# Kernel tuning notes

Hardware: AMD Instinct MI355X
Metric: run time of the kernel (lower is better)

Reference implementation:

```python
import jax, jax.numpy as jnp
import numpy as np

B, D, N_NEG, MAX_N = 4096, 256, 32768, 16
NEG_INF = float(jnp.finfo(jnp.float32).min)

def _l2norm(x):
    return x / jnp.linalg.norm(x, axis=-1, keepdims=True)

def setup_inputs() -> dict:
    key = jax.random.key(0)
    kq, kp, kn = jax.random.split(key, 3)
    q_emb = _l2norm(jax.random.normal(kq, (B, D), dtype=jnp.float32))
    p_emb = _l2norm(jax.random.normal(kp, (B, D), dtype=jnp.float32))
    n_emb = _l2norm(jax.random.normal(kn, (N_NEG, D), dtype=jnp.float32))
    # ragged counts in [0,16], mean 8, summing exactly to N_NEG
    rng = np.random.default_rng(0)
    d = rng.integers(0, 9, size=B // 2)
    counts = np.concatenate([8 + d, 8 - d])
    rng.shuffle(counts)
    n_counts = jnp.asarray(counts, dtype=jnp.int32)
    log_tau = jnp.log(jnp.asarray(0.07, dtype=jnp.float32))
    return {"q_emb": q_emb, "p_emb": p_emb, "n_emb": n_emb,
            "n_counts": n_counts, "log_tau": log_tau}

def reference(q_emb, p_emb, n_emb, n_counts, log_tau):
    Bq = q_emb.shape[0]
    tau = jnp.clip(jnp.exp(log_tau), 1e-4, 1.0)
    sim = (q_emb @ p_emb.T) / tau                      # [B, B]
    n_sim = (q_emb @ n_emb.T) / tau                    # [B, N]
    # vectorized ragged packing: query i's negatives live at
    # n_sim[i, offset[i] : offset[i]+cnt[i]]
    offsets = jnp.cumsum(n_counts) - n_counts          # [B]
    col = offsets[:, None] + jnp.arange(MAX_N)[None, :]
    valid = jnp.arange(MAX_N)[None, :] < n_counts[:, None]
    gathered = jnp.take_along_axis(n_sim, jnp.clip(col, 0, n_sim.shape[1] - 1), axis=1)
    neg_cols = jnp.where(valid, gathered, NEG_INF)     # [B, MAX_N]
    full = jnp.concatenate([sim, neg_cols], axis=1)    # [B, B+MAX_N]
    labels = jnp.arange(Bq)
    logp_q = jax.nn.log_softmax(full, axis=-1)
    loss_q = -jnp.mean(jnp.take_along_axis(logp_q, labels[:, None], axis=1))
    logp_p = jax.nn.log_softmax(sim.T, axis=-1)
    loss_p = -jnp.mean(jnp.take_along_axis(logp_p, labels[:, None], axis=1))
    return (loss_q + loss_p) / 2.0
```

## Files before the change

### kernel.cpp

```cpp
#include <hip/hip_runtime.h>
#include <math.h>

#define BQ 4096
#define DD 256
#define NNEG 32768

typedef __bf16 bf16x8 __attribute__((ext_vector_type(8)));
typedef float f32x4 __attribute__((ext_vector_type(4)));

typedef const __attribute__((address_space(1))) void GvPtr;
typedef __attribute__((address_space(3))) void LdsPtr;


__device__ __forceinline__ float get_inv_tau(const float* __restrict__ lt) {
  float tau = __expf(lt[0]);
  tau = fminf(fmaxf(tau, 1e-4f), 1.0f);
  return 1.0f / tau;
}

__device__ __forceinline__ unsigned int f2bf(float f) {
  unsigned int u = __float_as_uint(f);
  u += 0x7FFFu + ((u >> 16) & 1u);
  return u >> 16;
}

__global__ __launch_bounds__(256) void cvtscan_kernel(
    const float* __restrict__ q, const float* __restrict__ p,
    const int* __restrict__ counts,
    ushort* __restrict__ qb, ushort* __restrict__ pb,
    int* __restrict__ owner, float* __restrict__ rowcol ) {
  __shared__ int wtot[4];
  const int t = threadIdx.x;
  if (blockIdx.x < 1024) {
    const int i = blockIdx.x * 256 + t;
    const int half = (BQ * DD) / 8;
    const float* src = (i < half) ? q : p;
    ushort* dst = (i < half) ? qb : pb;
    const int idx = (i < half) ? i : (i - half);
    const float4 a = *reinterpret_cast<const float4*>(&src[idx * 8]);
    const float4 b = *reinterpret_cast<const float4*>(&src[idx * 8 + 4]);
    uint4 o;
    o.x = f2bf(a.x) | (f2bf(a.y) << 16);
    o.y = f2bf(a.z) | (f2bf(a.w) << 16);
    o.z = f2bf(b.x) | (f2bf(b.y) << 16);
    o.w = f2bf(b.z) | (f2bf(b.w) << 16);
    *reinterpret_cast<uint4*>(&dst[idx * 8]) = o;
    return;
  }
  const int wid = t >> 6, lane = t & 63;
  const float4 z = {0.f, 0.f, 0.f, 0.f};
#pragma unroll
  for (int i = 0; i < 8; ++i) reinterpret_cast<float4*>(rowcol)[t * 8 + i] = z;

  int cl[16];
  int s = 0;
#pragma unroll
  for (int i = 0; i < 4; ++i) {
    const int4 c = reinterpret_cast<const int4*>(counts)[t * 4 + i];
    cl[4 * i + 0] = c.x; cl[4 * i + 1] = c.y; cl[4 * i + 2] = c.z; cl[4 * i + 3] = c.w;
    s += c.x + c.y + c.z + c.w;
  }
  int x = s;
#pragma unroll
  for (int off = 1; off < 64; off <<= 1) {
    const int v = __shfl_up(x, off);
    if (lane >= off) x += v;
  }
  if (lane == 63) wtot[wid] = x;
  __syncthreads();
  int base = 0;
  for (int w = 0; w < wid; ++w) base += wtot[w];
  int running = base + x - s;
#pragma unroll
  for (int k = 0; k < 16; ++k) {
    const int qi = 16 * t + k;
    for (int e = 0; e < cl[k]; ++e) owner[running + e] = qi;
    running += cl[k];
  }
}

__global__ __launch_bounds__(256) void simneg_kernel(
    const ushort* __restrict__ qb, const ushort* __restrict__ pb,
    const float* __restrict__ q, const float* __restrict__ n_emb,
    const int* __restrict__ owner, const float* __restrict__ logtau,
    float* __restrict__ row_sum, float* __restrict__ col_sum,
    float* __restrict__ diag) {
  __shared__ ushort As[2][128 * 32];
  __shared__ ushort Bs[2][128 * 32];

  const int tid = threadIdx.x;
  const float inv_tau = get_inv_tau(logtau);
  const int bid = (int)blockIdx.x;

  if (bid >= 1024) {
    const int j = (bid - 1024) * 32 + (tid >> 3);
    const int sl = tid & 7;
    const int ow = owner[j];
    const float4* nrow = reinterpret_cast<const float4*>(n_emb + (size_t)j * DD);
    const float4* qrow = reinterpret_cast<const float4*>(q + (size_t)ow * DD);
    float d0 = 0.f, d1 = 0.f;
#pragma unroll
    for (int t = 0; t < 8; t += 2) {
      const float4 n0 = nrow[sl + 8 * t];
      const float4 q0 = qrow[sl + 8 * t];
      const float4 n1 = nrow[sl + 8 * (t + 1)];
      const float4 q1 = qrow[sl + 8 * (t + 1)];
      d0 += q0.x * n0.x + q0.y * n0.y + q0.z * n0.z + q0.w * n0.w;
      d1 += q1.x * n1.x + q1.y * n1.y + q1.z * n1.z + q1.w * n1.w;
    }
    float d = d0 + d1;
    d += __shfl_xor(d, 1);
    d += __shfl_xor(d, 2);
    d += __shfl_xor(d, 4);
    if (sl == 0) atomicAdd(&row_sum[ow], __expf(d * inv_tau));
    return;
  }

  const int lane = tid & 63;
  const int wv = tid >> 6;
  const int wr = wv >> 1, wc = wv & 1;
  const int lrow = lane >> 4;
  const int lcol = lane & 15;

  const int swz = (bid & 7) * 128 + (bid >> 3);
  const int bx = swz & 31, by = swz >> 5;
  const int brow = by * 128, bcol = bx * 128;

  const int sr = tid >> 2;
  const int sc = (tid & 3) * 8;

  f32x4 acc[4][4];
#pragma unroll
  for (int i = 0; i < 4; ++i)
#pragma unroll
    for (int j = 0; j < 4; ++j) acc[i][j] = (f32x4){0.f, 0.f, 0.f, 0.f};

#define STAGE(buf, k0)                                                          \
  {                                                                             \
    _Pragma("unroll")                                                           \
    for (int i = 0; i < 2; ++i) {                                               \
      const ushort* ga = qb + (size_t)(brow + i * 64 + sr) * DD + (k0) + sc;    \
      __builtin_amdgcn_global_load_lds((GvPtr*)ga,                              \
          (LdsPtr*)(&As[buf][0] + i * 2048 + tid * 8), 16, 0, 0);               \
      const ushort* gb = pb + (size_t)(bcol + i * 64 + sr) * DD + (k0) + sc;    \
      __builtin_amdgcn_global_load_lds((GvPtr*)gb,                              \
          (LdsPtr*)(&Bs[buf][0] + i * 2048 + tid * 8), 16, 0, 0);               \
    }                                                                           \
  }

  STAGE(0, 0);
  __syncthreads();

#pragma unroll
  for (int t = 0; t < 8; ++t) {
    if (t < 7) STAGE((t + 1) & 1, (t + 1) * 32);
    const ushort* lA = &As[t & 1][0];
    const ushort* lB = &Bs[t & 1][0];
    bf16x8 a[4], b[4];
#pragma unroll
    for (int m = 0; m < 4; ++m)
      a[m] = *reinterpret_cast<const bf16x8*>(lA + (wr * 64 + m * 16 + lcol) * 32 + lrow * 8);
#pragma unroll
    for (int n = 0; n < 4; ++n)
      b[n] = *reinterpret_cast<const bf16x8*>(lB + (wc * 64 + n * 16 + lcol) * 32 + lrow * 8);
#pragma unroll
    for (int m = 0; m < 4; ++m)
#pragma unroll
      for (int n = 0; n < 4; ++n)
        acc[m][n] = __builtin_amdgcn_mfma_f32_16x16x32_bf16(a[m], b[n], acc[m][n], 0, 0, 0);
    __syncthreads();
  }
#undef STAGE

  const int arow0 = brow + wr * 64;
  const int bcol0 = bcol + wc * 64;
  float colp[4] = {0.f, 0.f, 0.f, 0.f};
#pragma unroll
  for (int mi = 0; mi < 4; ++mi) {
    float rowp[4] = {0.f, 0.f, 0.f, 0.f};
#pragma unroll
    for (int ni = 0; ni < 4; ++ni) {
      const f32x4 v = acc[mi][ni];
#pragma unroll
      for (int r = 0; r < 4; ++r) {
        const float sv = v[r] * inv_tau;
        const float e = __expf(sv);
        const int gr = arow0 + mi * 16 + lrow * 4 + r;
        const int gc = bcol0 + ni * 16 + lcol;
        if (gr == gc) diag[gr] = sv;
        rowp[r] += e;
        colp[ni] += e;
      }
    }
#pragma unroll
    for (int r = 0; r < 4; ++r) {
      float x = rowp[r];
      x += __shfl_xor(x, 1);
      x += __shfl_xor(x, 2);
      x += __shfl_xor(x, 4);
      x += __shfl_xor(x, 8);
      if (lcol == 0) atomicAdd(&row_sum[arow0 + mi * 16 + lrow * 4 + r], x);
    }
  }
#pragma unroll
  for (int ni = 0; ni < 4; ++ni) {
    float x = colp[ni];
    x += __shfl_xor(x, 16);
    x += __shfl_xor(x, 32);
    if (lrow == 0) atomicAdd(&col_sum[bcol0 + ni * 16 + lcol], x);
  }
}

__global__ __launch_bounds__(1024) void finalize_kernel(
    const float* __restrict__ row_sum, const float* __restrict__ col_sum,
    const float* __restrict__ diag, float* __restrict__ out) {
  __shared__ float ws[16];
  const int t = threadIdx.x;
  const int wid = t >> 6, lane = t & 63;
  const float4 r = reinterpret_cast<const float4*>(row_sum)[t];
  const float4 c = reinterpret_cast<const float4*>(col_sum)[t];
  const float4 d = reinterpret_cast<const float4*>(diag)[t];
  float v = __logf(r.x) + __logf(r.y) + __logf(r.z) + __logf(r.w)
          + __logf(c.x) + __logf(c.y) + __logf(c.z) + __logf(c.w)
          - 2.f * (d.x + d.y + d.z + d.w);
  v += __shfl_xor(v, 1);
  v += __shfl_xor(v, 2);
  v += __shfl_xor(v, 4);
  v += __shfl_xor(v, 8);
  v += __shfl_xor(v, 16);
  v += __shfl_xor(v, 32);
  if (lane == 0) ws[wid] = v;
  __syncthreads();
  if (wid == 0) {
    float x = (lane < 16) ? ws[lane] : 0.f;
    x += __shfl_xor(x, 1);
    x += __shfl_xor(x, 2);
    x += __shfl_xor(x, 4);
    x += __shfl_xor(x, 8);
    if (lane == 0) out[0] = x / (2.0f * BQ);
  }
}

extern "C" void kernel_launch(void* const* d_in, const int* in_sizes, int n_in,
                              void* d_out, int out_size, void* d_ws, size_t ws_size,
                              hipStream_t stream) {
  const float* q      = (const float*)d_in[0];
  const float* p      = (const float*)d_in[1];
  const float* n_emb  = (const float*)d_in[2];
  const int*   counts = (const int*)d_in[3];
  const float* logtau = (const float*)d_in[4];
  float* out = (float*)d_out;

  float* ws      = (float*)d_ws;
  float* row_sum = ws;
  float* col_sum = ws + BQ;
  float* diag    = ws + 2 * BQ;
  int*   owner   = (int*)(ws + 3 * BQ);
  ushort* qb     = (ushort*)(owner + NNEG);
  ushort* pb     = qb + (size_t)BQ * DD;

  cvtscan_kernel<<<1025, 256, 0, stream>>>(q, p, counts, qb, pb, owner, row_sum);
  simneg_kernel<<<2048, 256, 0, stream>>>(qb, pb, q, n_emb, owner, logtau,
                                          row_sum, col_sum, diag);
  finalize_kernel<<<1, 1024, 0, stream>>>(row_sum, col_sum, diag, out);
}
```

Measured before the change: 137.8 us.

## Fuse bf16 conversion and scan into GEMM kernel, replace atomics with partials

Removes the separate convert/scan kernel. The GEMM blocks now load fp32 q/p directly, convert to bf16 in registers and write them to a swizzled LDS layout. Negative blocks recompute the prefix scan in LDS and find each row's owning query by binary search. Row and column sums, plus the per-negative exp values, are written to non-atomic partial buffers that the single finalize block reduces. This saves a launch and the bf16 round trip through global memory, but the staging becomes register-based instead of direct global-to-LDS loads, and the finalize block has much more reduction work to do.

```diff
diff --git a/kernel.cpp b/kernel.cpp
--- a/kernel.cpp
+++ b/kernel.cpp
@@ -7,9 +7,6 @@
 
 typedef __bf16 bf16x8 __attribute__((ext_vector_type(8)));
 typedef float f32x4 __attribute__((ext_vector_type(4)));
-
-typedef const __attribute__((address_space(1))) void GvPtr;
-typedef __attribute__((address_space(3))) void LdsPtr;
 
 
 __device__ __forceinline__ float get_inv_tau(const float* __restrict__ lt) {
@@ -23,88 +20,70 @@
   u += 0x7FFFu + ((u >> 16) & 1u);
   return u >> 16;
 }
-
-__global__ __launch_bounds__(256) void cvtscan_kernel(
+__device__ __forceinline__ unsigned int pack2(float a, float b) {
+  return f2bf(a) | (f2bf(b) << 16);
+}
+
+__global__ __launch_bounds__(256) void simneg_kernel(
     const float* __restrict__ q, const float* __restrict__ p,
-    const int* __restrict__ counts,
-    ushort* __restrict__ qb, ushort* __restrict__ pb,
-    int* __restrict__ owner, float* __restrict__ rowcol ) {
+    const float* __restrict__ n_emb, const int* __restrict__ counts,
+    const float* __restrict__ logtau,
+    float* __restrict__ diag, float* __restrict__ rpart,
+    float* __restrict__ cpart, float* __restrict__ npart) {
+  __shared__ ushort As[2][8192];
   __shared__ int wtot[4];
-  const int t = threadIdx.x;
-  if (blockIdx.x < 1024) {
-    const int i = blockIdx.x * 256 + t;
-    const int half = (BQ * DD) / 8;
-    const float* src = (i < half) ? q : p;
-    ushort* dst = (i < half) ? qb : pb;
-    const int idx = (i < half) ? i : (i - half);
-    const float4 a = *reinterpret_cast<const float4*>(&src[idx * 8]);
-    const float4 b = *reinterpret_cast<const float4*>(&src[idx * 8 + 4]);
-    uint4 o;
-    o.x = f2bf(a.x) | (f2bf(a.y) << 16);
-    o.y = f2bf(a.z) | (f2bf(a.w) << 16);
-    o.z = f2bf(b.x) | (f2bf(b.y) << 16);
-    o.w = f2bf(b.z) | (f2bf(b.w) << 16);
-    *reinterpret_cast<uint4*>(&dst[idx * 8]) = o;
-    return;
-  }
-  const int wid = t >> 6, lane = t & 63;
-  const float4 z = {0.f, 0.f, 0.f, 0.f};
-#pragma unroll
-  for (int i = 0; i < 8; ++i) reinterpret_cast<float4*>(rowcol)[t * 8 + i] = z;
-
-  int cl[16];
-  int s = 0;
-#pragma unroll
-  for (int i = 0; i < 4; ++i) {
-    const int4 c = reinterpret_cast<const int4*>(counts)[t * 4 + i];
-    cl[4 * i + 0] = c.x; cl[4 * i + 1] = c.y; cl[4 * i + 2] = c.z; cl[4 * i + 3] = c.w;
-    s += c.x + c.y + c.z + c.w;
-  }
-  int x = s;
-#pragma unroll
-  for (int off = 1; off < 64; off <<= 1) {
-    const int v = __shfl_up(x, off);
-    if (lane >= off) x += v;
-  }
-  if (lane == 63) wtot[wid] = x;
-  __syncthreads();
-  int base = 0;
-  for (int w = 0; w < wid; ++w) base += wtot[w];
-  int running = base + x - s;
-#pragma unroll
-  for (int k = 0; k < 16; ++k) {
-    const int qi = 16 * t + k;
-    for (int e = 0; e < cl[k]; ++e) owner[running + e] = qi;
-    running += cl[k];
-  }
-}
-
-__global__ __launch_bounds__(256) void simneg_kernel(
-    const ushort* __restrict__ qb, const ushort* __restrict__ pb,
-    const float* __restrict__ q, const float* __restrict__ n_emb,
-    const int* __restrict__ owner, const float* __restrict__ logtau,
-    float* __restrict__ row_sum, float* __restrict__ col_sum,
-    float* __restrict__ diag) {
-  __shared__ ushort As[2][128 * 32];
-  __shared__ ushort Bs[2][128 * 32];
 
   const int tid = threadIdx.x;
+  const int bid = (int)blockIdx.x;
   const float inv_tau = get_inv_tau(logtau);
-  const int bid = (int)blockIdx.x;
 
   if (bid >= 1024) {
+    int* P = (int*)&As[0][0];
+    const int lane = tid & 63, wid = tid >> 6;
+    int cl[16];
+    int s = 0;
+#pragma unroll
+    for (int i = 0; i < 4; ++i) {
+      const int4 cc = reinterpret_cast<const int4*>(counts)[tid * 4 + i];
+      cl[4 * i + 0] = cc.x; cl[4 * i + 1] = cc.y;
+      cl[4 * i + 2] = cc.z; cl[4 * i + 3] = cc.w;
+    }
+    int run = 0;
+#pragma unroll
+    for (int k = 0; k < 16; ++k) { run += cl[k]; cl[k] = run; }
+    s = run;
+    int x = s;
+#pragma unroll
+    for (int off = 1; off < 64; off <<= 1) {
+      const int v = __shfl_up(x, off);
+      if (lane >= off) x += v;
+    }
+    if (lane == 63) wtot[wid] = x;
+    __syncthreads();
+    int base = 0;
+    for (int w = 0; w < wid; ++w) base += wtot[w];
+    base += x - s;
+#pragma unroll
+    for (int k = 0; k < 16; ++k) P[16 * tid + k] = base + cl[k];
+    __syncthreads();
+
     const int j = (bid - 1024) * 32 + (tid >> 3);
     const int sl = tid & 7;
-    const int ow = owner[j];
+    int lo = 0, hi = 4095;
+    while (lo < hi) {
+      const int mid = (lo + hi) >> 1;
+      if (P[mid] > j) hi = mid; else lo = mid + 1;
+    }
+    const int ow = lo;
     const float4* nrow = reinterpret_cast<const float4*>(n_emb + (size_t)j * DD);
     const float4* qrow = reinterpret_cast<const float4*>(q + (size_t)ow * DD);
     float d0 = 0.f, d1 = 0.f;
 #pragma unroll
-    for (int t = 0; t < 8; t += 2) {
-      const float4 n0 = nrow[sl + 8 * t];
-      const float4 q0 = qrow[sl + 8 * t];
-      const float4 n1 = nrow[sl + 8 * (t + 1)];
-      const float4 q1 = qrow[sl + 8 * (t + 1)];
+    for (int t2 = 0; t2 < 8; t2 += 2) {
+      const float4 n0 = nrow[sl + 8 * t2];
+      const float4 q0 = qrow[sl + 8 * t2];
+      const float4 n1 = nrow[sl + 8 * (t2 + 1)];
+      const float4 q1 = qrow[sl + 8 * (t2 + 1)];
       d0 += q0.x * n0.x + q0.y * n0.y + q0.z * n0.z + q0.w * n0.w;
       d1 += q1.x * n1.x + q1.y * n1.y + q1.z * n1.z + q1.w * n1.w;
     }
@@ -112,7 +91,7 @@
     d += __shfl_xor(d, 1);
     d += __shfl_xor(d, 2);
     d += __shfl_xor(d, 4);
-    if (sl == 0) atomicAdd(&row_sum[ow], __expf(d * inv_tau));
+    if (sl == 0) npart[j] = __expf(d * inv_tau);
     return;
   }
 
@@ -126,8 +105,12 @@
   const int bx = swz & 31, by = swz >> 5;
   const int brow = by * 128, bcol = bx * 128;
 
-  const int sr = tid >> 2;
-  const int sc = (tid & 3) * 8;
+  const int ra = tid & 127, ca = tid >> 7;
+  char* Ab = (char*)&As[0][0];
+  char* Bb = (char*)&As[1][0];
+  char* awr = Ab + ra * 128;
+  char* bwr = Bb + ra * 128;
+  const int wswz = (ra & 7) << 4;
 
   f32x4 acc[4][4];
 #pragma unroll
@@ -135,45 +118,67 @@
 #pragma unroll
     for (int j = 0; j < 4; ++j) acc[i][j] = (f32x4){0.f, 0.f, 0.f, 0.f};
 
-#define STAGE(buf, k0)                                                          \
-  {                                                                             \
-    _Pragma("unroll")                                                           \
-    for (int i = 0; i < 2; ++i) {                                               \
-      const ushort* ga = qb + (size_t)(brow + i * 64 + sr) * DD + (k0) + sc;    \
-      __builtin_amdgcn_global_load_lds((GvPtr*)ga,                              \
-          (LdsPtr*)(&As[buf][0] + i * 2048 + tid * 8), 16, 0, 0);               \
-      const ushort* gb = pb + (size_t)(bcol + i * 64 + sr) * DD + (k0) + sc;    \
-      __builtin_amdgcn_global_load_lds((GvPtr*)gb,                              \
-          (LdsPtr*)(&Bs[buf][0] + i * 2048 + tid * 8), 16, 0, 0);               \
-    }                                                                           \
-  }
-
-  STAGE(0, 0);
-  __syncthreads();
-
-#pragma unroll
-  for (int t = 0; t < 8; ++t) {
-    if (t < 7) STAGE((t + 1) & 1, (t + 1) * 32);
-    const ushort* lA = &As[t & 1][0];
-    const ushort* lB = &Bs[t & 1][0];
-    bf16x8 a[4], b[4];
-#pragma unroll
-    for (int m = 0; m < 4; ++m)
-      a[m] = *reinterpret_cast<const bf16x8*>(lA + (wr * 64 + m * 16 + lcol) * 32 + lrow * 8);
-#pragma unroll
-    for (int n = 0; n < 4; ++n)
-      b[n] = *reinterpret_cast<const bf16x8*>(lB + (wc * 64 + n * 16 + lcol) * 32 + lrow * 8);
-#pragma unroll
-    for (int m = 0; m < 4; ++m)
-#pragma unroll
-      for (int n = 0; n < 4; ++n)
-        acc[m][n] = __builtin_amdgcn_mfma_f32_16x16x32_bf16(a[m], b[n], acc[m][n], 0, 0, 0);
+  float4 sa[8], sb[8];
+#define LOAD(k0)                                                                 \
+  {                                                                              \
+    const float4* qs = (const float4*)(q + (size_t)(brow + ra) * DD + (k0) + ca * 32); \
+    const float4* ps = (const float4*)(p + (size_t)(bcol + ra) * DD + (k0) + ca * 32); \
+    _Pragma("unroll") for (int u = 0; u < 8; ++u) { sa[u] = qs[u]; sb[u] = ps[u]; } \
+  }
+
+#define WRITE()                                                                  \
+  {                                                                              \
+    _Pragma("unroll") for (int u = 0; u < 4; ++u) {                              \
+      uint4 w;                                                                   \
+      w.x = pack2(sa[2 * u].x, sa[2 * u].y);                                     \
+      w.y = pack2(sa[2 * u].z, sa[2 * u].w);                                     \
+      w.z = pack2(sa[2 * u + 1].x, sa[2 * u + 1].y);                             \
+      w.w = pack2(sa[2 * u + 1].z, sa[2 * u + 1].w);                             \
+      *(uint4*)(awr + ((ca * 64 + u * 16) ^ wswz)) = w;                          \
+      uint4 v2;                                                                  \
+      v2.x = pack2(sb[2 * u].x, sb[2 * u].y);                                    \
+      v2.y = pack2(sb[2 * u].z, sb[2 * u].w);                                    \
+      v2.z = pack2(sb[2 * u + 1].x, sb[2 * u + 1].y);                            \
+      v2.w = pack2(sb[2 * u + 1].z, sb[2 * u + 1].w);                            \
+      *(uint4*)(bwr + ((ca * 64 + u * 16) ^ wswz)) = v2;                         \
+    }                                                                            \
+  }
+
+  const int arow = wr * 64 + lcol;
+  const int brow_f = wc * 64 + lcol;
+  const int rswz = (lcol & 7) << 4;
+  const char* ard = Ab + arow * 128;
+  const char* brd = Bb + brow_f * 128;
+
+  LOAD(0);
+#pragma unroll
+  for (int t = 0; t < 4; ++t) {
+    if (t > 0) __syncthreads();
+    WRITE();
     __syncthreads();
-  }
-#undef STAGE
+    if (t < 3) LOAD((t + 1) * 64);
+#pragma unroll
+    for (int sub = 0; sub < 2; ++sub) {
+      const int rb = (sub * 64 + lrow * 16) ^ rswz;
+      bf16x8 af[4], bf[4];
+#pragma unroll
+      for (int m = 0; m < 4; ++m) af[m] = *(const bf16x8*)(ard + m * 2048 + rb);
+#pragma unroll
+      for (int n = 0; n < 4; ++n) bf[n] = *(const bf16x8*)(brd + n * 2048 + rb);
+#pragma unroll
+      for (int m = 0; m < 4; ++m)
+#pragma unroll
+        for (int n = 0; n < 4; ++n)
+          acc[m][n] = __builtin_amdgcn_mfma_f32_16x16x32_bf16(af[m], bf[n], acc[m][n], 0, 0, 0);
+    }
+  }
+#undef LOAD
+#undef WRITE
 
   const int arow0 = brow + wr * 64;
   const int bcol0 = bcol + wc * 64;
+  float* rp = rpart + (size_t)(bx * 2 + wc) * BQ;
+  float* cp = cpart + (size_t)(by * 2 + wr) * BQ;
   float colp[4] = {0.f, 0.f, 0.f, 0.f};
 #pragma unroll
   for (int mi = 0; mi < 4; ++mi) {
@@ -199,7 +204,7 @@
       x += __shfl_xor(x, 2);
       x += __shfl_xor(x, 4);
       x += __shfl_xor(x, 8);
-      if (lcol == 0) atomicAdd(&row_sum[arow0 + mi * 16 + lrow * 4 + r], x);
+      if (lcol == 0) rp[arow0 + mi * 16 + lrow * 4 + r] = x;
     }
   }
 #pragma unroll
@@ -207,37 +212,73 @@
     float x = colp[ni];
     x += __shfl_xor(x, 16);
     x += __shfl_xor(x, 32);
-    if (lrow == 0) atomicAdd(&col_sum[bcol0 + ni * 16 + lcol], x);
+    if (lrow == 0) cp[bcol0 + ni * 16 + lcol] = x;
   }
 }
 
 __global__ __launch_bounds__(1024) void finalize_kernel(
-    const float* __restrict__ row_sum, const float* __restrict__ col_sum,
-    const float* __restrict__ diag, float* __restrict__ out) {
-  __shared__ float ws[16];
-  const int t = threadIdx.x;
-  const int wid = t >> 6, lane = t & 63;
-  const float4 r = reinterpret_cast<const float4*>(row_sum)[t];
-  const float4 c = reinterpret_cast<const float4*>(col_sum)[t];
-  const float4 d = reinterpret_cast<const float4*>(diag)[t];
-  float v = __logf(r.x) + __logf(r.y) + __logf(r.z) + __logf(r.w)
-          + __logf(c.x) + __logf(c.y) + __logf(c.z) + __logf(c.w)
-          - 2.f * (d.x + d.y + d.z + d.w);
+    const int* __restrict__ counts, const float* __restrict__ diag,
+    const float* __restrict__ rpart, const float* __restrict__ cpart,
+    const float* __restrict__ npart, float* __restrict__ out) {
+  __shared__ int wtot[16];
+  __shared__ float wsum[16];
+  const int t = threadIdx.x, wid = t >> 6, lane = t & 63;
+
+  const int4 c = reinterpret_cast<const int4*>(counts)[t];
+  const int s = c.x + c.y + c.z + c.w;
+  int x = s;
+#pragma unroll
+  for (int off = 1; off < 64; off <<= 1) {
+    const int v = __shfl_up(x, off);
+    if (lane >= off) x += v;
+  }
+  if (lane == 63) wtot[wid] = x;
+  __syncthreads();
+  int base = 0;
+  for (int w = 0; w < wid; ++w) base += wtot[w];
+  base += x - s;
+
+  float r0 = 0, r1 = 0, r2 = 0, r3 = 0, c0 = 0, c1 = 0, c2 = 0, c3 = 0;
+#pragma unroll 8
+  for (int k = 0; k < 64; ++k) {
+    const float4 rv = reinterpret_cast<const float4*>(rpart)[k * 1024 + t];
+    const float4 cv = reinterpret_cast<const float4*>(cpart)[k * 1024 + t];
+    r0 += rv.x; r1 += rv.y; r2 += rv.z; r3 += rv.w;
+    c0 += cv.x; c1 += cv.y; c2 += cv.z; c3 += cv.w;
+  }
+  const float4 dg = reinterpret_cast<const float4*>(diag)[t];
+
+  float n0 = 0, n1 = 0, n2 = 0, n3 = 0;
+  {
+    int e = base;
+    for (int i = 0; i < c.x; ++i) n0 += npart[e + i];
+    e += c.x;
+    for (int i = 0; i < c.y; ++i) n1 += npart[e + i];
+    e += c.y;
+    for (int i = 0; i < c.z; ++i) n2 += npart[e + i];
+    e += c.z;
+    for (int i = 0; i < c.w; ++i) n3 += npart[e + i];
+  }
+
+  float v = __logf(r0 + n0) + __logf(c0) - 2.f * dg.x
+          + __logf(r1 + n1) + __logf(c1) - 2.f * dg.y
+          + __logf(r2 + n2) + __logf(c2) - 2.f * dg.z
+          + __logf(r3 + n3) + __logf(c3) - 2.f * dg.w;
   v += __shfl_xor(v, 1);
   v += __shfl_xor(v, 2);
   v += __shfl_xor(v, 4);
   v += __shfl_xor(v, 8);
   v += __shfl_xor(v, 16);
   v += __shfl_xor(v, 32);
-  if (lane == 0) ws[wid] = v;
+  if (lane == 0) wsum[wid] = v;
   __syncthreads();
   if (wid == 0) {
-    float x = (lane < 16) ? ws[lane] : 0.f;
-    x += __shfl_xor(x, 1);
-    x += __shfl_xor(x, 2);
-    x += __shfl_xor(x, 4);
-    x += __shfl_xor(x, 8);
-    if (lane == 0) out[0] = x / (2.0f * BQ);
+    float y = (lane < 16) ? wsum[lane] : 0.f;
+    y += __shfl_xor(y, 1);
+    y += __shfl_xor(y, 2);
+    y += __shfl_xor(y, 4);
+    y += __shfl_xor(y, 8);
+    if (lane == 0) out[0] = y / (2.0f * BQ);
   }
 }
 
@@ -251,16 +292,13 @@
   const float* logtau = (const float*)d_in[4];
   float* out = (float*)d_out;
 
-  float* ws      = (float*)d_ws;
-  float* row_sum = ws;
-  float* col_sum = ws + BQ;
-  float* diag    = ws + 2 * BQ;
-  int*   owner   = (int*)(ws + 3 * BQ);
-  ushort* qb     = (ushort*)(owner + NNEG);
-  ushort* pb     = qb + (size_t)BQ * DD;
-
-  cvtscan_kernel<<<1025, 256, 0, stream>>>(q, p, counts, qb, pb, owner, row_sum);
-  simneg_kernel<<<2048, 256, 0, stream>>>(qb, pb, q, n_emb, owner, logtau,
-                                          row_sum, col_sum, diag);
-  finalize_kernel<<<1, 1024, 0, stream>>>(row_sum, col_sum, diag, out);
-}
+  float* ws    = (float*)d_ws;
+  float* diag  = ws;
+  float* rpart = ws + BQ;
+  float* cpart = rpart + 64 * BQ;
+  float* npart = cpart + 64 * BQ;
+
+  simneg_kernel<<<2048, 256, 0, stream>>>(q, p, n_emb, counts, logtau,
+                                          diag, rpart, cpart, npart);
+  finalize_kernel<<<1, 1024, 0, stream>>>(counts, diag, rpart, cpart, npart, out);
+}
```

Result: slower. 171.4 us (+24.4%).
